# Kernel tuning notes

Hardware: AMD Instinct MI355X
Metric: run time of the kernel (lower is better)

Reference implementation:

```python
import jax, jax.numpy as jnp
import numpy as np

B, C, H, W = 4, 256, 64, 64
C4 = C // 4
EPS = 1e-5  # BatchNorm eps (torch default)


def setup_inputs() -> dict:
    key = jax.random.key(0)
    ks = jax.random.split(key, 24)
    rn = lambda k, s, sc=1.0: jax.random.normal(k, s, jnp.float32) * sc
    un = lambda k, s: jax.random.uniform(k, s, jnp.float32, 0.5, 1.5)
    return {
        "x1": rn(ks[0], (B, C, H, W)),
        "x2": rn(ks[1], (B, C, H, W)),
        "x3": rn(ks[2], (B, C, H, W)),
        # conv_n1: in_c -> in_c//4, 1x1 conv + BN(affine) params
        "w1": rn(ks[3], (C4, C), 0.05), "b1": rn(ks[4], (C4,), 0.05),
        "g1": 1.0 + rn(ks[5], (C4,), 0.05), "be1": rn(ks[6], (C4,), 0.05),
        "m1": rn(ks[7], (C4,), 0.05), "v1": un(ks[8], (C4,)),
        # conv_n2: in_c -> in_c//4
        "w2": rn(ks[9], (C4, C), 0.05), "b2": rn(ks[10], (C4,), 0.05),
        "g2": 1.0 + rn(ks[11], (C4,), 0.05), "be2": rn(ks[12], (C4,), 0.05),
        "m2": rn(ks[13], (C4,), 0.05), "v2": un(ks[14], (C4,)),
        # conv_n3: in_c -> in_c
        "w3": rn(ks[15], (C, C), 0.05), "b3": rn(ks[16], (C,), 0.05),
        "g3": 1.0 + rn(ks[17], (C,), 0.05), "be3": rn(ks[18], (C,), 0.05),
        "m3": rn(ks[19], (C,), 0.05), "v3": un(ks[20], (C,)),
        # gamma residual gate (torch inits to 0; use 0.5 so the attention path matters)
        "gam": jnp.full((1,), 0.5, jnp.float32),
    }


def _cbr(x, w, b, g, be, m, v):
    # 1x1 conv == channel contraction, then inference-mode BN, then ReLU
    y = jnp.einsum("bchw,oc->bohw", x, w) + b[None, :, None, None]
    scale = (g * jax.lax.rsqrt(v + EPS))[None, :, None, None]
    shift = (be - g * m * jax.lax.rsqrt(v + EPS))[None, :, None, None]
    return jax.nn.relu(y * scale + shift)


def reference(x1, x2, x3,
              w1, b1, g1, be1, m1, v1,
              w2, b2, g2, be2, m2, v2,
              w3, b3, g3, be3, m3, v3,
              gam):
    b, c, h, w = x1.shape
    hw = h * w
    q = _cbr(x1, w1, b1, g1, be1, m1, v1).reshape(b, -1, hw).transpose(0, 2, 1)  # (b, hw, c/4)
    k = _cbr(x2, w2, b2, g2, be2, m2, v2).reshape(b, -1, hw)                      # (b, c/4, hw)
    attn = jax.nn.softmax(jnp.einsum("bnc,bcm->bnm", q, k), axis=-1)              # (b, hw, hw)
    val = _cbr(x3, w3, b3, g3, be3, m3, v3).reshape(b, c, hw)                     # (b, c, hw)
    # out[b,c,i] = sum_j val[b,c,j] * attn[b,i,j]   (bmm with attn^T)
    out = jnp.einsum("bcj,bij->bci", val, attn).reshape(b, c, h, w)
    return gam[0] * out + x1
```

## Files before the change

kernel.cpp:

```cpp
#include <hip/hip_runtime.h>
#include <math.h>

#define HW 4096
#define CIN 256
#define BN_EPS 1e-5f
#define LOG2E 1.44269504088896f

typedef __attribute__((ext_vector_type(8))) short short8;
typedef __attribute__((ext_vector_type(4))) float floatx4;
typedef __attribute__((ext_vector_type(4))) unsigned short u16x4;
typedef unsigned short ushort;
typedef unsigned int u32;

__device__ inline ushort f2bf(float f) {
    union { float f; unsigned u; } c; c.f = f;
    unsigned r = c.u + 0x7fff + ((c.u >> 16) & 1);
    return (ushort)(r >> 16);
}
__device__ inline float bf2f(ushort u) {
    union { unsigned u; float f; } c; c.u = ((u32)u) << 16; return c.f;
}

__device__ inline void load_lds16(const ushort* g, ushort* l) {
    __builtin_amdgcn_global_load_lds(
        (const __attribute__((address_space(1))) u32*)g,
        (__attribute__((address_space(3))) u32*)l, 16, 0, 0);
}

__global__ __launch_bounds__(256) void transpose_bf16(
    const float* __restrict__ x1, const float* __restrict__ x2,
    const float* __restrict__ x3, ushort* __restrict__ Xt1,
    ushort* __restrict__ Xt2, ushort* __restrict__ Xt3)
{
    const int z = blockIdx.z;
    const int inp = z >> 2, b = z & 3;
    const float* x = inp == 0 ? x1 : (inp == 1 ? x2 : x3);
    ushort* o = inp == 0 ? Xt1 : (inp == 1 ? Xt2 : Xt3);
    const int c0 = blockIdx.y << 6, p0 = blockIdx.x << 6;
    const int tid = threadIdx.x;

    __shared__ float t[64 * 65];

    const int col = tid & 63, r4 = tid >> 6;
#pragma unroll
    for (int t2 = 0; t2 < 16; t2++) {
        int row = (t2 << 2) + r4;
        t[row * 65 + col] = x[((size_t)(b * CIN + c0 + row) << 12) + p0 + col];
    }
    __syncthreads();
    const int p = tid >> 2, cs = (tid & 3) << 4;
    alignas(16) ushort v[16];
#pragma unroll
    for (int k = 0; k < 16; k++) v[k] = f2bf(t[(cs + k) * 65 + p]);
    size_t base = ((size_t)(b * HW + p0 + p)) * 256 + c0 + cs;
    *(short8*)&o[base]     = *(short8*)&v[0];
    *(short8*)&o[base + 8] = *(short8*)&v[8];
}

__global__ __launch_bounds__(256) void prep_weights(
    const float* __restrict__ w1, const float* __restrict__ b1,
    const float* __restrict__ g1, const float* __restrict__ be1,
    const float* __restrict__ m1, const float* __restrict__ v1,
    const float* __restrict__ w2, const float* __restrict__ b2,
    const float* __restrict__ g2, const float* __restrict__ be2,
    const float* __restrict__ m2, const float* __restrict__ v2,
    const float* __restrict__ w3, const float* __restrict__ b3,
    const float* __restrict__ g3, const float* __restrict__ be3,
    const float* __restrict__ m3, const float* __restrict__ v3,
    ushort* __restrict__ w1c, ushort* __restrict__ w2c, ushort* __restrict__ w3c,
    float* __restrict__ bc)
{
    const int bid = blockIdx.x, tid = threadIdx.x;
    if (bid < 384) {
        int idx = bid * 256 + tid;
        if (idx < 16384) {
            int o = idx >> 8;
            float A = g1[o] * rsqrtf(v1[o] + BN_EPS) * LOG2E;
            w1c[idx] = f2bf(w1[idx] * A);
        } else if (idx < 32768) {
            int i2 = idx - 16384, o = i2 >> 8;
            float A = g2[o] * rsqrtf(v2[o] + BN_EPS);
            w2c[i2] = f2bf(w2[i2] * A);
        } else {
            int i3 = idx - 32768, o = i3 >> 8;
            float A = g3[o] * rsqrtf(v3[o] + BN_EPS);
            w3c[i3] = f2bf(w3[i3] * A);
        }
    } else {
        if (tid < 64) {
            float A = g1[tid] * rsqrtf(v1[tid] + BN_EPS);
            bc[tid] = ((b1[tid] - m1[tid]) * A + be1[tid]) * LOG2E;
        } else if (tid < 128) {
            int o = tid - 64;
            float A = g2[o] * rsqrtf(v2[o] + BN_EPS);
            bc[tid] = (b2[o] - m2[o]) * A + be2[o];
        } else {
#pragma unroll
            for (int t = 0; t < 2; t++) {
                int o = (tid - 128) + t * 128;
                float A = g3[o] * rsqrtf(v3[o] + BN_EPS);
                bc[128 + o] = (b3[o] - m3[o]) * A + be3[o];
            }
        }
    }
}

__global__ __launch_bounds__(256) void gemm_qk(
    const ushort* __restrict__ Xt1, const ushort* __restrict__ Xt2,
    const ushort* __restrict__ w1c, const ushort* __restrict__ w2c,
    const float* __restrict__ bc, ushort* __restrict__ Qw, ushort* __restrict__ Kw)
{
    const int which = blockIdx.z;
    const ushort* X = which ? Xt2 : Xt1;
    const ushort* W = which ? w2c : w1c;
    const float* bias = bc + which * 64;
    ushort* out = which ? Kw : Qw;
    const int b = blockIdx.y;
    const int px0 = blockIdx.x << 6;

    __shared__ alignas(16) ushort Wl[64 * 64];
    __shared__ alignas(16) ushort Xl[64 * 64];

    const int tid = threadIdx.x;
    const int lane = tid & 63;
    const int wv = tid >> 6;
    const int l15 = lane & 15, qd = lane >> 4;
    const int n0w = wv << 4;
    const int sw = l15 & 7;

    floatx4 acc[4];
#pragma unroll
    for (int mt = 0; mt < 4; mt++) acc[mt] = (floatx4){0.f, 0.f, 0.f, 0.f};

    for (int kk = 0; kk < 4; kk++) {
        const int k0 = kk << 6;
        __syncthreads();
#pragma unroll
        for (int t = 0; t < 2; t++) {
            int L = t * 256 + tid;
            int row = L >> 3, c = L & 7;
            load_lds16(W + row * 256 + k0 + ((c ^ (row & 7)) << 3), Wl + L * 8);
            load_lds16(X + ((size_t)(b * HW + px0 + row)) * 256 + k0 + ((c ^ (row & 7)) << 3),
                       Xl + L * 8);
        }
        __syncthreads();
#pragma unroll
        for (int kb = 0; kb < 2; kb++) {
            const int csel = (((kb << 2) + qd) ^ sw) << 3;
            short8 bfr = *(const short8*)&Xl[((n0w + l15) << 6) + csel];
#pragma unroll
            for (int mt = 0; mt < 4; mt++) {
                short8 af = *(const short8*)&Wl[(((mt << 4) + l15) << 6) + csel];
                acc[mt] = __builtin_amdgcn_mfma_f32_16x16x32_bf16(af, bfr, acc[mt], 0, 0, 0);
            }
        }
    }
    const int px = px0 + n0w + l15;
#pragma unroll
    for (int mt = 0; mt < 4; mt++) {
        alignas(8) ushort v4[4];
#pragma unroll
        for (int r = 0; r < 4; r++) {
            int oc = (mt << 4) + (qd << 2) + r;
            v4[r] = f2bf(fmaxf(acc[mt][r] + bias[oc], 0.f));
        }
        *(u16x4*)&out[(((size_t)(b * HW + px)) << 6) + (mt << 4) + (qd << 2)] = *(u16x4*)v4;
    }
}

__global__ __launch_bounds__(256) void gemm_v(
    const ushort* __restrict__ Xt3, const ushort* __restrict__ w3c,
    const float* __restrict__ bc, ushort* __restrict__ Vw)
{
    const int b = blockIdx.y;
    const int px0 = blockIdx.x << 6;
    const int oc0 = blockIdx.z << 7;
    const float* bias = bc + 128;

    __shared__ alignas(16) ushort Xl[64 * 64];
    __shared__ alignas(16) ushort Wl[128 * 64];

    const int tid = threadIdx.x;
    const int lane = tid & 63;
    const int wv = tid >> 6;
    const int l15 = lane & 15, qd = lane >> 4;
    const int wm0 = (wv & 1) << 5, wn0 = (wv >> 1) << 6;
    const int sw = l15 & 7;

    floatx4 acc[2][4];
#pragma unroll
    for (int mt = 0; mt < 2; mt++)
#pragma unroll
        for (int nt = 0; nt < 4; nt++) acc[mt][nt] = (floatx4){0.f, 0.f, 0.f, 0.f};

    for (int kk = 0; kk < 4; kk++) {
        const int k0 = kk << 6;
        __syncthreads();
#pragma unroll
        for (int t = 0; t < 2; t++) {
            int L = t * 256 + tid;
            int row = L >> 3, c = L & 7;
            load_lds16(Xt3 + ((size_t)(b * HW + px0 + row)) * 256 + k0 + ((c ^ (row & 7)) << 3),
                       Xl + L * 8);
        }
#pragma unroll
        for (int t = 0; t < 4; t++) {
            int L = t * 256 + tid;
            int row = L >> 3, c = L & 7;
            load_lds16(w3c + (oc0 + row) * 256 + k0 + ((c ^ (row & 7)) << 3), Wl + L * 8);
        }
        __syncthreads();
#pragma unroll
        for (int kb = 0; kb < 2; kb++) {
            const int csel = (((kb << 2) + qd) ^ sw) << 3;
            short8 af[2], bfr[4];
#pragma unroll
            for (int mt = 0; mt < 2; mt++)
                af[mt] = *(const short8*)&Xl[((wm0 + (mt << 4) + l15) << 6) + csel];
#pragma unroll
            for (int nt = 0; nt < 4; nt++)
                bfr[nt] = *(const short8*)&Wl[((wn0 + (nt << 4) + l15) << 6) + csel];
#pragma unroll
            for (int mt = 0; mt < 2; mt++)
#pragma unroll
                for (int nt = 0; nt < 4; nt++)
                    acc[mt][nt] = __builtin_amdgcn_mfma_f32_16x16x32_bf16(
                        af[mt], bfr[nt], acc[mt][nt], 0, 0, 0);
        }
    }
#pragma unroll
    for (int nt = 0; nt < 4; nt++) {
        int oc = oc0 + wn0 + (nt << 4) + l15;
        float bv = bias[oc];
#pragma unroll
        for (int mt = 0; mt < 2; mt++) {
            alignas(8) ushort v4[4];
#pragma unroll
            for (int r = 0; r < 4; r++)
                v4[r] = f2bf(fmaxf(acc[mt][nt][r] + bv, 0.f));
            size_t base = (((size_t)(b * CIN + oc)) << 12) + px0 + wm0 + (mt << 4) + (qd << 2);
            *(u16x4*)&Vw[base] = *(u16x4*)v4;
        }
    }
}

__global__ __launch_bounds__(512, 4) void flash_mfma(
    const ushort* __restrict__ Q, const ushort* __restrict__ K,
    const ushort* __restrict__ Vtg, ushort* __restrict__ Op0,
    ushort* __restrict__ Op1, float* __restrict__ mlM, float* __restrict__ mlL)
{
    const int tid = threadIdx.x;
    const int lane = tid & 63;
    const int wv = tid >> 6;
    const int it = wv & 3, ch = wv >> 2;
    const int l15 = lane & 15, qd = lane >> 4;
    const int sw = l15 & 7;

    const int bid = blockIdx.x;
    const int s = bid >> 8;
    const int r8 = bid & 255;
    const int b = (r8 & 7) >> 1;
    const int itile = ((r8 >> 3) << 1) | (r8 & 1);
    const int i0 = itile << 6;
    const int jbeg = s << 11;

    __shared__ alignas(16) ushort Kt[64 * 64];
    __shared__ alignas(16) ushort Vt[256 * 64];
    __shared__ alignas(16) ushort Pt[64 * 64];

    const int prow = it * 16 + l15;

    short8 qf[2];
#pragma unroll
    for (int kb = 0; kb < 2; kb++)
        qf[kb] = *(const short8*)(Q + (((size_t)((b << 12) + i0 + prow)) << 6) + kb * 32 + qd * 8);

    const floatx4 zv = {0.f, 0.f, 0.f, 0.f};
    floatx4 acc[8];
#pragma unroll
    for (int ct = 0; ct < 8; ct++) acc[ct] = zv;
    float mrun = -3.0e38f, lrun = 0.f;

    for (int jj = 0; jj < 2048; jj += 64) {
        const int j0 = jbeg + jj;
        __syncthreads();
        {
            int row = tid >> 3, cb = tid & 7;
            load_lds16(K + (((size_t)((b << 12) + j0 + row)) << 6) + ((cb ^ (row & 7)) << 3),
                       Kt + tid * 8);
#pragma unroll
            for (int t2 = 0; t2 < 4; t2++) {
                int idx = tid + (t2 << 9);
                int vr = idx >> 3, vc = idx & 7;
                load_lds16(Vtg + (((size_t)(b * CIN + vr)) << 12) + j0 + ((vc ^ (vr & 7)) << 3),
                           Vt + idx * 8);
            }
        }
        __syncthreads();

        floatx4 st[4];
#pragma unroll
        for (int t = 0; t < 4; t++) st[t] = zv;
#pragma unroll
        for (int kb = 0; kb < 2; kb++) {
            const int csel = (((kb << 2) + qd) ^ sw) << 3;
#pragma unroll
            for (int t = 0; t < 4; t++) {
                short8 kf = *(const short8*)&Kt[(((t << 4) + l15) << 6) + csel];
                st[t] = __builtin_amdgcn_mfma_f32_16x16x32_bf16(kf, qf[kb], st[t], 0, 0, 0);
            }
        }

        float mloc = -3.0e38f;
#pragma unroll
        for (int t = 0; t < 4; t++)
#pragma unroll
            for (int r = 0; r < 4; r++) mloc = fmaxf(mloc, st[t][r]);
        mloc = fmaxf(mloc, __shfl_xor(mloc, 16));
        mloc = fmaxf(mloc, __shfl_xor(mloc, 32));
        float mnew = fmaxf(mrun, mloc);

        float rs = 0.f;
#pragma unroll
        for (int t = 0; t < 4; t++)
#pragma unroll
            for (int r = 0; r < 4; r++) {
                float p = exp2f(st[t][r] - mnew);
                st[t][r] = p;
                rs += p;
            }
        rs += __shfl_xor(rs, 16);
        rs += __shfl_xor(rs, 32);
        float alpha = exp2f(mrun - mnew);
        mrun = mnew;
        lrun = lrun * alpha + rs;

        if (ch == 0) {
#pragma unroll
            for (int t = 0; t < 4; t++) {
                u16x4 pk;
#pragma unroll
                for (int r = 0; r < 4; r++) pk[r] = f2bf(st[t][r]);
                int jb8 = (t << 1) + (qd >> 1);
                *(u16x4*)&Pt[(prow << 6) + (((jb8 ^ sw) << 3) + ((qd & 1) << 2))] = pk;
            }
        }
        __syncthreads();

        if (__any(alpha < 1.0f)) {
#pragma unroll
            for (int ct = 0; ct < 8; ct++) acc[ct] *= alpha;
        }

        short8 pf[2];
#pragma unroll
        for (int kb = 0; kb < 2; kb++)
            pf[kb] = *(const short8*)&Pt[(prow << 6) + ((((kb << 2) + qd) ^ sw) << 3)];
#pragma unroll
        for (int kb = 0; kb < 2; kb++) {
            const int csel = (((kb << 2) + qd) ^ sw) << 3;
#pragma unroll
            for (int ct = 0; ct < 8; ct++) {
                int crow = (ch << 7) + (ct << 4) + l15;
                short8 vf = *(const short8*)&Vt[(crow << 6) + csel];
                acc[ct] = __builtin_amdgcn_mfma_f32_16x16x32_bf16(vf, pf[kb], acc[ct], 0, 0, 0);
            }
        }
    }

    ushort* Op = s ? Op1 : Op0;
    size_t obase = ((size_t)((b << 12) + i0 + prow)) << 8;
#pragma unroll
    for (int ct = 0; ct < 8; ct++) {
        u16x4 pk;
#pragma unroll
        for (int r = 0; r < 4; r++) pk[r] = f2bf(acc[ct][r]);
        *(u16x4*)&Op[obase + (ch << 7) + (ct << 4) + (qd << 2)] = pk;
    }
    if (ch == 0 && qd == 0) {
        int mi = (s << 14) + (b << 12) + i0 + prow;
        mlM[mi] = mrun;
        mlL[mi] = lrun;
    }
}

__global__ __launch_bounds__(256) void merge_out(
    const ushort* __restrict__ Op0, const ushort* __restrict__ Op1,
    const float* __restrict__ mlM, const float* __restrict__ mlL,
    const float* __restrict__ x1, const float* __restrict__ gam,
    float* __restrict__ out)
{
    const int b = blockIdx.z, c0 = blockIdx.y << 6, i0 = blockIdx.x << 6;
    const int tid = threadIdx.x;

    __shared__ float Tl[64][65];
    __shared__ float a0s[64], a1s[64];

    if (tid < 64) {
        int gi = (b << 12) + i0 + tid;
        float m0 = mlM[gi], m1 = mlM[16384 + gi];
        float l0 = mlL[gi], l1 = mlL[16384 + gi];
        float M = fmaxf(m0, m1);
        float w0 = exp2f(m0 - M), w1 = exp2f(m1 - M);
        float gd = gam[0] / (w0 * l0 + w1 * l1);
        a0s[tid] = w0 * gd;
        a1s[tid] = w1 * gd;
    }
    __syncthreads();
#pragma unroll
    for (int k = 0; k < 4; k++) {
        int idx4 = tid + (k << 8);
        int i = idx4 >> 4, c4 = (idx4 & 15) << 2;
        size_t g = ((size_t)((b << 12) + i0 + i)) * 256 + c0 + c4;
        u16x4 p0 = *(const u16x4*)&Op0[g];
        u16x4 p1 = *(const u16x4*)&Op1[g];
        float A0 = a0s[i], A1 = a1s[i];
#pragma unroll
        for (int r = 0; r < 4; r++)
            Tl[c4 + r][i] = A0 * bf2f(p0[r]) + A1 * bf2f(p1[r]);
    }
    __syncthreads();
#pragma unroll
    for (int k = 0; k < 4; k++) {
        int idx4 = tid + (k << 8);
        int c = idx4 >> 4, i4 = (idx4 & 15) << 2;
        size_t g = (((size_t)(b * CIN + c0 + c)) << 12) + i0 + i4;
        float4 xv = *(const float4*)&x1[g];
        float4 o;
        o.x = Tl[c][i4 + 0] + xv.x;
        o.y = Tl[c][i4 + 1] + xv.y;
        o.z = Tl[c][i4 + 2] + xv.z;
        o.w = Tl[c][i4 + 3] + xv.w;
        *(float4*)&out[g] = o;
    }
}

extern "C" void kernel_launch(void* const* d_in, const int* in_sizes, int n_in,
                              void* d_out, int out_size, void* d_ws, size_t ws_size,
                              hipStream_t stream)
{
    const float* x1  = (const float*)d_in[0];
    const float* x2  = (const float*)d_in[1];
    const float* x3  = (const float*)d_in[2];
    const float* w1  = (const float*)d_in[3];
    const float* b1  = (const float*)d_in[4];
    const float* g1  = (const float*)d_in[5];
    const float* be1 = (const float*)d_in[6];
    const float* m1  = (const float*)d_in[7];
    const float* v1  = (const float*)d_in[8];
    const float* w2  = (const float*)d_in[9];
    const float* b2  = (const float*)d_in[10];
    const float* g2  = (const float*)d_in[11];
    const float* be2 = (const float*)d_in[12];
    const float* m2  = (const float*)d_in[13];
    const float* v2  = (const float*)d_in[14];
    const float* w3  = (const float*)d_in[15];
    const float* b3  = (const float*)d_in[16];
    const float* g3  = (const float*)d_in[17];
    const float* be3 = (const float*)d_in[18];
    const float* m3  = (const float*)d_in[19];
    const float* v3  = (const float*)d_in[20];
    const float* gam = (const float*)d_in[21];

    ushort* Xt1 = (ushort*)d_ws;
    ushort* Xt2 = Xt1 + (size_t)4194304;
    ushort* Xt3 = Xt2 + (size_t)4194304;
    ushort* Qw  = Xt3 + (size_t)4194304;
    ushort* Kw  = Qw  + (size_t)1048576;
    ushort* Vw  = Kw  + (size_t)1048576;
    ushort* w1c = Vw  + (size_t)4194304;
    ushort* w2c = w1c + 16384;
    ushort* w3c = w2c + 16384;
    float*  bc  = (float*)(w3c + 65536);

    ushort* Op0 = Xt1;
    ushort* Op1 = Xt2;
    float*  mlM = (float*)Xt3;
    float*  mlL = mlM + 32768;

    transpose_bf16<<<dim3(64, 4, 12), 256, 0, stream>>>(x1, x2, x3, Xt1, Xt2, Xt3);
    prep_weights<<<385, 256, 0, stream>>>(w1, b1, g1, be1, m1, v1,
                                          w2, b2, g2, be2, m2, v2,
                                          w3, b3, g3, be3, m3, v3,
                                          w1c, w2c, w3c, bc);
    gemm_qk<<<dim3(64, 4, 2), 256, 0, stream>>>(Xt1, Xt2, w1c, w2c, bc, Qw, Kw);
    gemm_v <<<dim3(64, 4, 2), 256, 0, stream>>>(Xt3, w3c, bc, Vw);
    flash_mfma<<<512, 512, 0, stream>>>(Qw, Kw, Vw, Op0, Op1, mlM, mlL);
    merge_out<<<dim3(64, 4, 4), 256, 0, stream>>>(Op0, Op1, mlM, mlL, x1, gam, (float*)d_out);
}
```

Before: 240.2 us.

## Fuse input transpose into GEMMs, use Cauchy-Schwarz softmax bound, double-buffer flash

```diff
diff --git a/kernel.cpp b/kernel.cpp
--- a/kernel.cpp
+++ b/kernel.cpp
@@ -25,36 +25,6 @@
     __builtin_amdgcn_global_load_lds(
         (const __attribute__((address_space(1))) u32*)g,
         (__attribute__((address_space(3))) u32*)l, 16, 0, 0);
-}
-
-__global__ __launch_bounds__(256) void transpose_bf16(
-    const float* __restrict__ x1, const float* __restrict__ x2,
-    const float* __restrict__ x3, ushort* __restrict__ Xt1,
-    ushort* __restrict__ Xt2, ushort* __restrict__ Xt3)
-{
-    const int z = blockIdx.z;
-    const int inp = z >> 2, b = z & 3;
-    const float* x = inp == 0 ? x1 : (inp == 1 ? x2 : x3);
-    ushort* o = inp == 0 ? Xt1 : (inp == 1 ? Xt2 : Xt3);
-    const int c0 = blockIdx.y << 6, p0 = blockIdx.x << 6;
-    const int tid = threadIdx.x;
-
-    __shared__ float t[64 * 65];
-
-    const int col = tid & 63, r4 = tid >> 6;
-#pragma unroll
-    for (int t2 = 0; t2 < 16; t2++) {
-        int row = (t2 << 2) + r4;
-        t[row * 65 + col] = x[((size_t)(b * CIN + c0 + row) << 12) + p0 + col];
-    }
-    __syncthreads();
-    const int p = tid >> 2, cs = (tid & 3) << 4;
-    alignas(16) ushort v[16];
-#pragma unroll
-    for (int k = 0; k < 16; k++) v[k] = f2bf(t[(cs + k) * 65 + p]);
-    size_t base = ((size_t)(b * HW + p0 + p)) * 256 + c0 + cs;
-    *(short8*)&o[base]     = *(short8*)&v[0];
-    *(short8*)&o[base + 8] = *(short8*)&v[8];
 }
 
 __global__ __launch_bounds__(256) void prep_weights(
@@ -68,7 +38,7 @@
     const float* __restrict__ g3, const float* __restrict__ be3,
     const float* __restrict__ m3, const float* __restrict__ v3,
     ushort* __restrict__ w1c, ushort* __restrict__ w2c, ushort* __restrict__ w3c,
-    float* __restrict__ bc)
+    float* __restrict__ bc, unsigned* __restrict__ KmxU)
 {
     const int bid = blockIdx.x, tid = threadIdx.x;
     if (bid < 384) {
@@ -87,6 +57,7 @@
             w3c[i3] = f2bf(w3[i3] * A);
         }
     } else {
+        if (tid < 4) KmxU[tid] = 0u;
         if (tid < 64) {
             float A = g1[tid] * rsqrtf(v1[tid] + BN_EPS);
             bc[tid] = ((b1[tid] - m1[tid]) * A + be1[tid]) * LOG2E;
@@ -106,31 +77,33 @@
 }
 
 __global__ __launch_bounds__(256) void gemm_qk(
-    const ushort* __restrict__ Xt1, const ushort* __restrict__ Xt2,
+    const float* __restrict__ x1, const float* __restrict__ x2,
     const ushort* __restrict__ w1c, const ushort* __restrict__ w2c,
-    const float* __restrict__ bc, ushort* __restrict__ Qw, ushort* __restrict__ Kw)
+    const float* __restrict__ bc, ushort* __restrict__ Qw, ushort* __restrict__ Kw,
+    float* __restrict__ Qn, unsigned* __restrict__ KmxU)
 {
     const int which = blockIdx.z;
-    const ushort* X = which ? Xt2 : Xt1;
+    const float* x = which ? x2 : x1;
     const ushort* W = which ? w2c : w1c;
     const float* bias = bc + which * 64;
     ushort* out = which ? Kw : Qw;
     const int b = blockIdx.y;
-    const int px0 = blockIdx.x << 6;
+    const int px0 = blockIdx.x << 7;
 
     __shared__ alignas(16) ushort Wl[64 * 64];
-    __shared__ alignas(16) ushort Xl[64 * 64];
+    __shared__ alignas(16) float Xf[64 * 132];
+    __shared__ float redn[128];
 
     const int tid = threadIdx.x;
     const int lane = tid & 63;
     const int wv = tid >> 6;
     const int l15 = lane & 15, qd = lane >> 4;
-    const int n0w = wv << 4;
-    const int sw = l15 & 7;
-
-    floatx4 acc[4];
-#pragma unroll
-    for (int mt = 0; mt < 4; mt++) acc[mt] = (floatx4){0.f, 0.f, 0.f, 0.f};
+
+    floatx4 acc[4][2];
+#pragma unroll
+    for (int mt = 0; mt < 4; mt++)
+#pragma unroll
+        for (int nt = 0; nt < 2; nt++) acc[mt][nt] = (floatx4){0.f, 0.f, 0.f, 0.f};
 
     for (int kk = 0; kk < 4; kk++) {
         const int k0 = kk << 6;
@@ -138,58 +111,98 @@
 #pragma unroll
         for (int t = 0; t < 2; t++) {
             int L = t * 256 + tid;
-            int row = L >> 3, c = L & 7;
-            load_lds16(W + row * 256 + k0 + ((c ^ (row & 7)) << 3), Wl + L * 8);
-            load_lds16(X + ((size_t)(b * HW + px0 + row)) * 256 + k0 + ((c ^ (row & 7)) << 3),
-                       Xl + L * 8);
+            int row = L >> 3, c8 = L & 7;
+            load_lds16(W + row * 256 + k0 + ((c8 ^ (row & 7)) << 3), Wl + L * 8);
+        }
+#pragma unroll
+        for (int t = 0; t < 8; t++) {
+            int idx = t * 256 + tid;
+            int row = idx >> 5, p4 = (idx & 31) << 2;
+            *(float4*)&Xf[row * 132 + p4] =
+                *(const float4*)&x[((size_t)(b * CIN + k0 + row) << 12) + px0 + p4];
         }
         __syncthreads();
 #pragma unroll
         for (int kb = 0; kb < 2; kb++) {
-            const int csel = (((kb << 2) + qd) ^ sw) << 3;
-            short8 bfr = *(const short8*)&Xl[((n0w + l15) << 6) + csel];
+            short8 af[4], bfr[2];
 #pragma unroll
             for (int mt = 0; mt < 4; mt++) {
-                short8 af = *(const short8*)&Wl[(((mt << 4) + l15) << 6) + csel];
-                acc[mt] = __builtin_amdgcn_mfma_f32_16x16x32_bf16(af, bfr, acc[mt], 0, 0, 0);
-            }
-        }
-    }
-    const int px = px0 + n0w + l15;
-#pragma unroll
-    for (int mt = 0; mt < 4; mt++) {
-        alignas(8) ushort v4[4];
-#pragma unroll
-        for (int r = 0; r < 4; r++) {
-            int oc = (mt << 4) + (qd << 2) + r;
-            v4[r] = f2bf(fmaxf(acc[mt][r] + bias[oc], 0.f));
-        }
-        *(u16x4*)&out[(((size_t)(b * HW + px)) << 6) + (mt << 4) + (qd << 2)] = *(u16x4*)v4;
+                int row = (mt << 4) + l15;
+                af[mt] = *(const short8*)&Wl[(row << 6) + ((((kb << 2) + qd) ^ (row & 7)) << 3)];
+            }
+#pragma unroll
+            for (int nt = 0; nt < 2; nt++) {
+                int pxl = (wv << 5) + (nt << 4) + l15;
+                alignas(16) ushort tmp[8];
+#pragma unroll
+                for (int j = 0; j < 8; j++)
+                    tmp[j] = f2bf(Xf[((kb << 5) + (qd << 3) + j) * 132 + pxl]);
+                bfr[nt] = *(short8*)tmp;
+            }
+#pragma unroll
+            for (int mt = 0; mt < 4; mt++)
+#pragma unroll
+                for (int nt = 0; nt < 2; nt++)
+                    acc[mt][nt] = __builtin_amdgcn_mfma_f32_16x16x32_bf16(
+                        af[mt], bfr[nt], acc[mt][nt], 0, 0, 0);
+        }
+    }
+#pragma unroll
+    for (int nt = 0; nt < 2; nt++) {
+        int px = px0 + (wv << 5) + (nt << 4) + l15;
+        float s2 = 0.f;
+#pragma unroll
+        for (int mt = 0; mt < 4; mt++) {
+            alignas(8) ushort v4[4];
+#pragma unroll
+            for (int r = 0; r < 4; r++) {
+                int oc = (mt << 4) + (qd << 2) + r;
+                float y = fmaxf(acc[mt][nt][r] + bias[oc], 0.f);
+                s2 += y * y;
+                v4[r] = f2bf(y);
+            }
+            *(u16x4*)&out[(((size_t)(b * HW + px)) << 6) + (mt << 4) + (qd << 2)] = *(u16x4*)v4;
+        }
+        s2 += __shfl_xor(s2, 16);
+        s2 += __shfl_xor(s2, 32);
+        if (which == 0) {
+            if (qd == 0) Qn[(b << 12) + px] = sqrtf(s2);
+        } else {
+            if (qd == 0) redn[(wv << 5) + (nt << 4) + l15] = s2;
+        }
+    }
+    if (which == 1) {
+        __syncthreads();
+        if (tid < 128) {
+            float v = redn[tid];
+#pragma unroll
+            for (int off = 1; off < 64; off <<= 1) v = fmaxf(v, __shfl_xor(v, off));
+            if ((tid & 63) == 0) atomicMax(&KmxU[b], __float_as_uint(sqrtf(v)));
+        }
     }
 }
 
 __global__ __launch_bounds__(256) void gemm_v(
-    const ushort* __restrict__ Xt3, const ushort* __restrict__ w3c,
+    const float* __restrict__ x3, const ushort* __restrict__ w3c,
     const float* __restrict__ bc, ushort* __restrict__ Vw)
 {
     const int b = blockIdx.y;
-    const int px0 = blockIdx.x << 6;
+    const int px0 = blockIdx.x << 7;
     const int oc0 = blockIdx.z << 7;
     const float* bias = bc + 128;
 
-    __shared__ alignas(16) ushort Xl[64 * 64];
+    __shared__ alignas(16) float Xf[64 * 132];
     __shared__ alignas(16) ushort Wl[128 * 64];
 
     const int tid = threadIdx.x;
     const int lane = tid & 63;
     const int wv = tid >> 6;
     const int l15 = lane & 15, qd = lane >> 4;
-    const int wm0 = (wv & 1) << 5, wn0 = (wv >> 1) << 6;
-    const int sw = l15 & 7;
-
-    floatx4 acc[2][4];
-#pragma unroll
-    for (int mt = 0; mt < 2; mt++)
+    const int wm0 = (wv & 1) << 6, wn0 = (wv >> 1) << 6;
+
+    floatx4 acc[4][4];
+#pragma unroll
+    for (int mt = 0; mt < 4; mt++)
 #pragma unroll
         for (int nt = 0; nt < 4; nt++) acc[mt][nt] = (floatx4){0.f, 0.f, 0.f, 0.f};
 
@@ -197,31 +210,38 @@
         const int k0 = kk << 6;
         __syncthreads();
 #pragma unroll
-        for (int t = 0; t < 2; t++) {
-            int L = t * 256 + tid;
-            int row = L >> 3, c = L & 7;
-            load_lds16(Xt3 + ((size_t)(b * HW + px0 + row)) * 256 + k0 + ((c ^ (row & 7)) << 3),
-                       Xl + L * 8);
-        }
-#pragma unroll
         for (int t = 0; t < 4; t++) {
             int L = t * 256 + tid;
-            int row = L >> 3, c = L & 7;
-            load_lds16(w3c + (oc0 + row) * 256 + k0 + ((c ^ (row & 7)) << 3), Wl + L * 8);
+            int row = L >> 3, c8 = L & 7;
+            load_lds16(w3c + (oc0 + row) * 256 + k0 + ((c8 ^ (row & 7)) << 3), Wl + L * 8);
+        }
+#pragma unroll
+        for (int t = 0; t < 8; t++) {
+            int idx = t * 256 + tid;
+            int row = idx >> 5, p4 = (idx & 31) << 2;
+            *(float4*)&Xf[row * 132 + p4] =
+                *(const float4*)&x3[((size_t)(b * CIN + k0 + row) << 12) + px0 + p4];
         }
         __syncthreads();
 #pragma unroll
         for (int kb = 0; kb < 2; kb++) {
-            const int csel = (((kb << 2) + qd) ^ sw) << 3;
-            short8 af[2], bfr[4];
-#pragma unroll
-            for (int mt = 0; mt < 2; mt++)
-                af[mt] = *(const short8*)&Xl[((wm0 + (mt << 4) + l15) << 6) + csel];
-#pragma unroll
-            for (int nt = 0; nt < 4; nt++)
-                bfr[nt] = *(const short8*)&Wl[((wn0 + (nt << 4) + l15) << 6) + csel];
-#pragma unroll
-            for (int mt = 0; mt < 2; mt++)
+            short8 af[4], bfr[4];
+#pragma unroll
+            for (int mt = 0; mt < 4; mt++) {
+                int pxl = wm0 + (mt << 4) + l15;
+                alignas(16) ushort tmp[8];
+#pragma unroll
+                for (int j = 0; j < 8; j++)
+                    tmp[j] = f2bf(Xf[((kb << 5) + (qd << 3) + j) * 132 + pxl]);
+                af[mt] = *(short8*)tmp;
+            }
+#pragma unroll
+            for (int nt = 0; nt < 4; nt++) {
+                int row = wn0 + (nt << 4) + l15;
+                bfr[nt] = *(const short8*)&Wl[(row << 6) + ((((kb << 2) + qd) ^ (row & 7)) << 3)];
+            }
+#pragma unroll
+            for (int mt = 0; mt < 4; mt++)
 #pragma unroll
                 for (int nt = 0; nt < 4; nt++)
                     acc[mt][nt] = __builtin_amdgcn_mfma_f32_16x16x32_bf16(
@@ -233,7 +253,7 @@
         int oc = oc0 + wn0 + (nt << 4) + l15;
         float bv = bias[oc];
 #pragma unroll
-        for (int mt = 0; mt < 2; mt++) {
+        for (int mt = 0; mt < 4; mt++) {
             alignas(8) ushort v4[4];
 #pragma unroll
             for (int r = 0; r < 4; r++)
@@ -244,143 +264,136 @@
     }
 }
 
-__global__ __launch_bounds__(512, 4) void flash_mfma(
+__global__ __launch_bounds__(512, 2) void flash_mfma(
     const ushort* __restrict__ Q, const ushort* __restrict__ K,
-    const ushort* __restrict__ Vtg, ushort* __restrict__ Op0,
+    const ushort* __restrict__ Vtg, const float* __restrict__ Qn,
+    const unsigned* __restrict__ KmxU, ushort* __restrict__ Op0,
     ushort* __restrict__ Op1, float* __restrict__ mlM, float* __restrict__ mlL)
 {
     const int tid = threadIdx.x;
     const int lane = tid & 63;
     const int wv = tid >> 6;
-    const int it = wv & 3, ch = wv >> 2;
+    const int iw = wv & 1, ch = wv >> 1;
     const int l15 = lane & 15, qd = lane >> 4;
     const int sw = l15 & 7;
 
     const int bid = blockIdx.x;
-    const int s = bid >> 8;
-    const int r8 = bid & 255;
-    const int b = (r8 & 7) >> 1;
-    const int itile = ((r8 >> 3) << 1) | (r8 & 1);
-    const int i0 = itile << 6;
+    const int s = bid & 1;
+    const int b = (bid >> 1) & 3;
+    const int it = bid >> 3;
+    const int i0 = it << 7;
     const int jbeg = s << 11;
 
-    __shared__ alignas(16) ushort Kt[64 * 64];
-    __shared__ alignas(16) ushort Vt[256 * 64];
-    __shared__ alignas(16) ushort Pt[64 * 64];
-
-    const int prow = it * 16 + l15;
+    __shared__ alignas(16) ushort KV[2][20480];
+    __shared__ alignas(16) ushort Pt[128 * 64];
+
+    const float kmx = __uint_as_float(KmxU[b]);
+    const int iS = i0 + (wv << 4) + l15;
+    const float Mi = Qn[(b << 12) + iS] * kmx;
 
     short8 qf[2];
 #pragma unroll
     for (int kb = 0; kb < 2; kb++)
-        qf[kb] = *(const short8*)(Q + (((size_t)((b << 12) + i0 + prow)) << 6) + kb * 32 + qd * 8);
+        qf[kb] = *(const short8*)(Q + (((size_t)((b << 12) + iS)) << 6) + kb * 32 + qd * 8);
 
     const floatx4 zv = {0.f, 0.f, 0.f, 0.f};
-    floatx4 acc[8];
-#pragma unroll
-    for (int ct = 0; ct < 8; ct++) acc[ct] = zv;
-    float mrun = -3.0e38f, lrun = 0.f;
-
-    for (int jj = 0; jj < 2048; jj += 64) {
-        const int j0 = jbeg + jj;
-        __syncthreads();
-        {
-            int row = tid >> 3, cb = tid & 7;
-            load_lds16(K + (((size_t)((b << 12) + j0 + row)) << 6) + ((cb ^ (row & 7)) << 3),
-                       Kt + tid * 8);
-#pragma unroll
-            for (int t2 = 0; t2 < 4; t2++) {
-                int idx = tid + (t2 << 9);
-                int vr = idx >> 3, vc = idx & 7;
-                load_lds16(Vtg + (((size_t)(b * CIN + vr)) << 12) + j0 + ((vc ^ (vr & 7)) << 3),
-                           Vt + idx * 8);
-            }
-        }
-        __syncthreads();
+    floatx4 acc[4][4];
+#pragma unroll
+    for (int ct = 0; ct < 4; ct++)
+#pragma unroll
+        for (int is = 0; is < 4; is++) acc[ct][is] = zv;
+    float lsum = 0.f;
+
+#define STAGE(BUF, J0)                                                           \
+    {                                                                            \
+        int row = tid >> 3, c8 = tid & 7;                                        \
+        load_lds16(K + (((size_t)((b << 12) + (J0) + row)) << 6) +               \
+                       ((c8 ^ (row & 7)) << 3), KV[BUF] + tid * 8);              \
+        _Pragma("unroll")                                                        \
+        for (int t2 = 0; t2 < 4; t2++) {                                         \
+            int idx = tid + (t2 << 9);                                           \
+            int vr = idx >> 3, vc = idx & 7;                                     \
+            load_lds16(Vtg + (((size_t)((b << 8) + vr)) << 12) + (J0) +          \
+                           ((vc ^ (vr & 7)) << 3), KV[BUF] + 4096 + idx * 8);    \
+        }                                                                        \
+    }
+
+    STAGE(0, jbeg)
+
+    for (int jj = 0; jj < 32; jj++) {
+        __syncthreads();
+        const ushort* Kt = KV[jj & 1];
+        const ushort* Vt = KV[jj & 1] + 4096;
 
         floatx4 st[4];
 #pragma unroll
-        for (int t = 0; t < 4; t++) st[t] = zv;
+        for (int jt = 0; jt < 4; jt++) st[jt] = zv;
 #pragma unroll
         for (int kb = 0; kb < 2; kb++) {
             const int csel = (((kb << 2) + qd) ^ sw) << 3;
 #pragma unroll
-            for (int t = 0; t < 4; t++) {
-                short8 kf = *(const short8*)&Kt[(((t << 4) + l15) << 6) + csel];
-                st[t] = __builtin_amdgcn_mfma_f32_16x16x32_bf16(kf, qf[kb], st[t], 0, 0, 0);
-            }
-        }
-
-        float mloc = -3.0e38f;
-#pragma unroll
-        for (int t = 0; t < 4; t++)
-#pragma unroll
-            for (int r = 0; r < 4; r++) mloc = fmaxf(mloc, st[t][r]);
-        mloc = fmaxf(mloc, __shfl_xor(mloc, 16));
-        mloc = fmaxf(mloc, __shfl_xor(mloc, 32));
-        float mnew = fmaxf(mrun, mloc);
-
-        float rs = 0.f;
-#pragma unroll
-        for (int t = 0; t < 4; t++)
-#pragma unroll
-            for (int r = 0; r < 4; r++) {
-                float p = exp2f(st[t][r] - mnew);
-                st[t][r] = p;
-                rs += p;
-            }
-        rs += __shfl_xor(rs, 16);
-        rs += __shfl_xor(rs, 32);
-        float alpha = exp2f(mrun - mnew);
-        mrun = mnew;
-        lrun = lrun * alpha + rs;
-
-        if (ch == 0) {
-#pragma unroll
-            for (int t = 0; t < 4; t++) {
-                u16x4 pk;
-#pragma unroll
-                for (int r = 0; r < 4; r++) pk[r] = f2bf(st[t][r]);
-                int jb8 = (t << 1) + (qd >> 1);
-                *(u16x4*)&Pt[(prow << 6) + (((jb8 ^ sw) << 3) + ((qd & 1) << 2))] = pk;
-            }
-        }
-        __syncthreads();
-
-        if (__any(alpha < 1.0f)) {
-#pragma unroll
-            for (int ct = 0; ct < 8; ct++) acc[ct] *= alpha;
-        }
-
-        short8 pf[2];
-#pragma unroll
-        for (int kb = 0; kb < 2; kb++)
-            pf[kb] = *(const short8*)&Pt[(prow << 6) + ((((kb << 2) + qd) ^ sw) << 3)];
+            for (int jt = 0; jt < 4; jt++) {
+                short8 kf = *(const short8*)&Kt[(((jt << 4) + l15) << 6) + csel];
+                st[jt] = __builtin_amdgcn_mfma_f32_16x16x32_bf16(kf, qf[kb], st[jt], 0, 0, 0);
+            }
+        }
+
+        const int prow = (wv << 4) + l15;
+#pragma unroll
+        for (int jt = 0; jt < 4; jt++) {
+            float p0 = exp2f(st[jt][0] - Mi);
+            float p1 = exp2f(st[jt][1] - Mi);
+            float p2 = exp2f(st[jt][2] - Mi);
+            float p3 = exp2f(st[jt][3] - Mi);
+            lsum += (p0 + p1) + (p2 + p3);
+            alignas(8) ushort pk[4] = {f2bf(p0), f2bf(p1), f2bf(p2), f2bf(p3)};
+            int c8 = (jt << 1) + (qd >> 1);
+            *(u16x4*)&Pt[(prow << 6) + ((c8 ^ (prow & 7)) << 3) + ((qd & 1) << 2)] =
+                *(u16x4*)pk;
+        }
+        __syncthreads();
+
+        if (jj + 1 < 32) STAGE((jj + 1) & 1, jbeg + ((jj + 1) << 6))
+
 #pragma unroll
         for (int kb = 0; kb < 2; kb++) {
             const int csel = (((kb << 2) + qd) ^ sw) << 3;
-#pragma unroll
-            for (int ct = 0; ct < 8; ct++) {
-                int crow = (ch << 7) + (ct << 4) + l15;
-                short8 vf = *(const short8*)&Vt[(crow << 6) + csel];
-                acc[ct] = __builtin_amdgcn_mfma_f32_16x16x32_bf16(vf, pf[kb], acc[ct], 0, 0, 0);
-            }
-        }
-    }
+            short8 pf[4];
+#pragma unroll
+            for (int is = 0; is < 4; is++)
+                pf[is] = *(const short8*)&Pt[(((iw << 6) + (is << 4) + l15) << 6) + csel];
+#pragma unroll
+            for (int ct = 0; ct < 4; ct++) {
+                short8 vf = *(const short8*)&Vt[(((ch << 6) + (ct << 4) + l15) << 6) + csel];
+#pragma unroll
+                for (int is = 0; is < 4; is++)
+                    acc[ct][is] = __builtin_amdgcn_mfma_f32_16x16x32_bf16(
+                        vf, pf[is], acc[ct][is], 0, 0, 0);
+            }
+        }
+    }
+#undef STAGE
+
+    lsum += __shfl_xor(lsum, 16);
+    lsum += __shfl_xor(lsum, 32);
 
     ushort* Op = s ? Op1 : Op0;
-    size_t obase = ((size_t)((b << 12) + i0 + prow)) << 8;
-#pragma unroll
-    for (int ct = 0; ct < 8; ct++) {
-        u16x4 pk;
-#pragma unroll
-        for (int r = 0; r < 4; r++) pk[r] = f2bf(acc[ct][r]);
-        *(u16x4*)&Op[obase + (ch << 7) + (ct << 4) + (qd << 2)] = pk;
-    }
-    if (ch == 0 && qd == 0) {
-        int mi = (s << 14) + (b << 12) + i0 + prow;
-        mlM[mi] = mrun;
-        mlL[mi] = lrun;
+#pragma unroll
+    for (int is = 0; is < 4; is++) {
+        int i = i0 + (iw << 6) + (is << 4) + l15;
+        size_t obase = (((size_t)((b << 12) + i)) << 8);
+#pragma unroll
+        for (int ct = 0; ct < 4; ct++) {
+            alignas(8) ushort pk[4];
+#pragma unroll
+            for (int r = 0; r < 4; r++) pk[r] = f2bf(acc[ct][is][r]);
+            *(u16x4*)&Op[obase + (ch << 6) + (ct << 4) + (qd << 2)] = *(u16x4*)pk;
+        }
+    }
+    if (qd == 0) {
+        int mi2 = (s << 14) + (b << 12) + iS;
+        mlM[mi2] = Mi;
+        mlL[mi2] = lsum;
     }
 }
 
@@ -462,29 +475,26 @@
     const float* v3  = (const float*)d_in[20];
     const float* gam = (const float*)d_in[21];
 
-    ushort* Xt1 = (ushort*)d_ws;
-    ushort* Xt2 = Xt1 + (size_t)4194304;
-    ushort* Xt3 = Xt2 + (size_t)4194304;
-    ushort* Qw  = Xt3 + (size_t)4194304;
+    ushort* Qw  = (ushort*)d_ws;
     ushort* Kw  = Qw  + (size_t)1048576;
     ushort* Vw  = Kw  + (size_t)1048576;
     ushort* w1c = Vw  + (size_t)4194304;
     ushort* w2c = w1c + 16384;
     ushort* w3c = w2c + 16384;
     float*  bc  = (float*)(w3c + 65536);
-
-    ushort* Op0 = Xt1;
-    ushort* Op1 = Xt2;
-    float*  mlM = (float*)Xt3;
+    float*  Qn  = bc + 384;
+    unsigned* KmxU = (unsigned*)(Qn + 16384);
+    ushort* Op0 = (ushort*)(KmxU + 4);
+    ushort* Op1 = Op0 + (size_t)4194304;
+    float*  mlM = (float*)(Op1 + (size_t)4194304);
     float*  mlL = mlM + 32768;
 
-    transpose_bf16<<<dim3(64, 4, 12), 256, 0, stream>>>(x1, x2, x3, Xt1, Xt2, Xt3);
     prep_weights<<<385, 256, 0, stream>>>(w1, b1, g1, be1, m1, v1,
                                           w2, b2, g2, be2, m2, v2,
                                           w3, b3, g3, be3, m3, v3,
-                                          w1c, w2c, w3c, bc);
-    gemm_qk<<<dim3(64, 4, 2), 256, 0, stream>>>(Xt1, Xt2, w1c, w2c, bc, Qw, Kw);
-    gemm_v <<<dim3(64, 4, 2), 256, 0, stream>>>(Xt3, w3c, bc, Vw);
-    flash_mfma<<<512, 512, 0, stream>>>(Qw, Kw, Vw, Op0, Op1, mlM, mlL);
+                                          w1c, w2c, w3c, bc, KmxU);
+    gemm_qk<<<dim3(32, 4, 2), 256, 0, stream>>>(x1, x2, w1c, w2c, bc, Qw, Kw, Qn, KmxU);
+    gemm_v <<<dim3(32, 4, 2), 256, 0, stream>>>(x3, w3c, bc, Vw);
+    flash_mfma<<<256, 512, 0, stream>>>(Qw, Kw, Vw, Qn, KmxU, Op0, Op1, mlM, mlL);
     merge_out<<<dim3(64, 4, 4), 256, 0, stream>>>(Op0, Op1, mlM, mlL, x1, gam, (float*)d_out);
 }
```

New measurement: 241.0 us. About the same (+0.3%).
